# Kernel tuning notes

Hardware: AMD Instinct MI355X
Metric: run time of the kernel (lower is better)

Reference implementation:

```python
import jax, jax.numpy as jnp
import numpy as np

N = 20000      # nodes
E = 320000     # edges
G = 512        # graphs in batch
F_IN = 64      # node_feature_dim
SOLV = 128     # solvent fingerprint dim
OUT = 1        # output_dim
EPS = 1e-5     # BatchNorm eps


def setup_inputs() -> dict:
    key = jax.random.key(0)
    ks = jax.random.split(key, 24)
    inp = {
        'x': jax.random.normal(ks[0], (N, F_IN), jnp.float32),
        'edge_index': jax.random.randint(ks[1], (2, E), 0, N),
        'batch': jnp.sort(jax.random.randint(ks[2], (N,), 0, G)),
        'solvent_fingerprint': jax.random.normal(ks[3], (G, SOLV), jnp.float32),
        # GCNConv 1: 64 -> 128
        'W1': jax.random.normal(ks[4], (F_IN, 128), jnp.float32) / np.sqrt(F_IN),
        'b1': jnp.zeros((128,), jnp.float32),
        'g1': 1.0 + 0.1 * jax.random.normal(ks[5], (128,), jnp.float32),
        'be1': 0.1 * jax.random.normal(ks[6], (128,), jnp.float32),
        # GCNConv 2: 128 -> 256
        'W2': jax.random.normal(ks[7], (128, 256), jnp.float32) / np.sqrt(128),
        'b2': jnp.zeros((256,), jnp.float32),
        'g2': 1.0 + 0.1 * jax.random.normal(ks[8], (256,), jnp.float32),
        'be2': 0.1 * jax.random.normal(ks[9], (256,), jnp.float32),
        # fc_solvent: 128 -> 128
        'Ws': jax.random.normal(ks[10], (SOLV, 128), jnp.float32) / np.sqrt(SOLV),
        'bs': jnp.zeros((128,), jnp.float32),
        # fc1: 384 -> 128 (+ BN)
        'Wf1': jax.random.normal(ks[11], (384, 128), jnp.float32) / np.sqrt(384),
        'bf1': jnp.zeros((128,), jnp.float32),
        'gf1': 1.0 + 0.1 * jax.random.normal(ks[12], (128,), jnp.float32),
        'bef1': 0.1 * jax.random.normal(ks[13], (128,), jnp.float32),
        # fc2: 128 -> OUT
        'Wf2': jax.random.normal(ks[14], (128, OUT), jnp.float32) / np.sqrt(128),
        'bf2': jnp.zeros((OUT,), jnp.float32),
    }
    return inp


def _batchnorm(h, g, b):
    # training-mode BatchNorm1d: biased batch statistics
    mu = jnp.mean(h, axis=0)
    var = jnp.var(h, axis=0)
    return g * (h - mu) * jax.lax.rsqrt(var + EPS) + b


def _gcn_norm(edge_index, n_nodes):
    # add self-loops, symmetric normalization (PyG GCNConv default)
    loops = jnp.arange(n_nodes)
    row = jnp.concatenate([edge_index[0], loops])
    col = jnp.concatenate([edge_index[1], loops])
    deg = jax.ops.segment_sum(jnp.ones_like(col, jnp.float32), col, num_segments=n_nodes)
    dis = jax.lax.rsqrt(deg)  # deg >= 1 due to self-loops
    norm = dis[row] * dis[col]  # [E+N]
    return row, col, norm


def _gcn_conv(h, W, b, row, col, norm, n_nodes):
    hw = h @ W                                   # [N, F_out]
    msg = hw[row] * norm[:, None]                # gather + scale
    agg = jax.ops.segment_sum(msg, col, num_segments=n_nodes)
    return agg + b


def reference(x, edge_index, batch, solvent_fingerprint,
              W1, b1, g1, be1, W2, b2, g2, be2,
              Ws, bs, Wf1, bf1, gf1, bef1, Wf2, bf2):
    n = x.shape[0]
    row, col, norm = _gcn_norm(edge_index, n)

    h = jax.nn.relu(_batchnorm(_gcn_conv(x, W1, b1, row, col, norm, n), g1, be1))
    h = jax.nn.relu(_batchnorm(_gcn_conv(h, W2, b2, row, col, norm, n), g2, be2))

    # global_mean_pool
    sums = jax.ops.segment_sum(h, batch, num_segments=G)
    cnts = jax.ops.segment_sum(jnp.ones((n,), h.dtype), batch, num_segments=G)
    pooled = sums / jnp.maximum(cnts, 1.0)[:, None]          # [G, 256]

    solv = jax.nn.relu(solvent_fingerprint @ Ws + bs)        # [G, 128]
    z = jnp.concatenate([pooled, solv], axis=1)              # [G, 384]
    z = jax.nn.relu(_batchnorm(z @ Wf1 + bf1, gf1, bef1))    # dropout = identity (eval)
    return z @ Wf2 + bf2                                     # [G, OUT]
```

## Files before the change

### kernel.cpp

```cpp
#include <hip/hip_runtime.h>
#include <hip/hip_bf16.h>
#include <hip/hip_fp16.h>

#define EPS 1e-5f
#define CAP 64

typedef __attribute__((ext_vector_type(8))) short short8_t;
typedef __attribute__((ext_vector_type(8))) unsigned short ushort8_t;
typedef __attribute__((ext_vector_type(4))) float f32x4_t;

__device__ inline unsigned short f2bf(float f) {
    unsigned int u = __float_as_uint(f);
    unsigned int r = (u + 0x7FFFu + ((u >> 16) & 1u)) >> 16;
    return (unsigned short)r;
}
__device__ inline float bf2f(unsigned short h) {
    return __uint_as_float((unsigned int)h << 16);
}

__global__ void prep_kernel(const float* __restrict__ x, unsigned short* __restrict__ xb,
                            int* __restrict__ cursor, float* __restrict__ st,
                            const int* __restrict__ batch, int* __restrict__ seg,
                            float* __restrict__ out, const float* __restrict__ bf2,
                            int n, int G) {
    int i = blockIdx.x * blockDim.x + threadIdx.x;
    if (i < n * 8) {
        const float4* xf4 = (const float4*)x;
        float4 u = xf4[i * 2];
        float4 v = xf4[i * 2 + 1];
        ushort8_t h;
        h[0] = f2bf(u.x); h[1] = f2bf(u.y); h[2] = f2bf(u.z); h[3] = f2bf(u.w);
        h[4] = f2bf(v.x); h[5] = f2bf(v.y); h[6] = f2bf(v.z); h[7] = f2bf(v.w);
        ((ushort8_t*)xb)[i] = h;
    }
    if (i < n) cursor[i] = 0;
    if (i < 1028) st[i] = 0.f;
    if (i < G) out[i] = bf2[0];
    if (i <= G) {
        if (i == G) { seg[G] = n; }
        else {
            int lo = 0, hi = n;
            while (lo < hi) {
                int mid = (lo + hi) >> 1;
                if (batch[mid] < i) lo = mid + 1; else hi = mid;
            }
            seg[i] = lo;
        }
    }
}

__global__ void fillb_kernel(const int* __restrict__ ei, int* __restrict__ cursor,
                             unsigned int* __restrict__ recs, int E) {
    int e = blockIdx.x * blockDim.x + threadIdx.x;
    if (e >= E) return;
    int r = ei[e];
    int c = ei[E + e];
    int pos = atomicAdd(&cursor[c], 1);
    recs[(size_t)c * CAP + pos] = (unsigned int)r;
}

__global__ __launch_bounds__(256)
void gather1_pack_kernel(const unsigned short* __restrict__ xb,
                         const int* __restrict__ cursor,
                         unsigned int* __restrict__ recs,
                         unsigned short* __restrict__ dst,
                         int n, int gps, int GB1) {
    const int bid = blockIdx.x;
    const int t   = threadIdx.x;

    if (bid >= GB1) {
        int i = (bid - GB1) * 256 + t;
        int node = i >> 6;
        if (node < n && (i & 63) < cursor[node]) {
            unsigned int r = recs[i] & 0xFFFFu;
            float w = rsqrtf((float)cursor[r] + 1.0f);
            recs[i] = (((unsigned int)__half_as_ushort(__float2half_rn(w))) << 16) | r;
        }
        return;
    }

    int xl    = bid & 7;
    int slice = xl >> 2;
    int group = (bid >> 3) * 4 + (xl & 3);
    if (group >= gps) return;
    int local = t / 4;
    int lane  = t % 4;
    int node  = group * 64 + local;
    if (node >= n) return;
    int f8    = slice * 4 + lane;

    const ushort8_t* src8 = (const ushort8_t*)xb;
    int deg  = cursor[node];
    float di = rsqrtf((float)deg + 1.0f);
    ushort8_t sv = src8[(size_t)node * 8 + f8];
    float acc[8], acc2[8];
#pragma unroll
    for (int j = 0; j < 8; j++) { acc[j] = bf2f(sv[j]) * di; acc2[j] = 0.f; }

    int e  = node * CAP;
    int e1 = e + deg;
    for (; e + 1 < e1; e += 2) {
        int r0 = recs[e] & 0xFFFF;
        int r1 = recs[e + 1] & 0xFFFF;
        float w0 = rsqrtf((float)cursor[r0] + 1.0f);
        float w1 = rsqrtf((float)cursor[r1] + 1.0f);
        ushort8_t v0 = src8[(size_t)r0 * 8 + f8];
        ushort8_t v1 = src8[(size_t)r1 * 8 + f8];
#pragma unroll
        for (int j = 0; j < 8; j++) {
            acc[j]  = fmaf(bf2f(v0[j]), w0, acc[j]);
            acc2[j] = fmaf(bf2f(v1[j]), w1, acc2[j]);
        }
    }
    if (e < e1) {
        int r0 = recs[e] & 0xFFFF;
        float w0 = rsqrtf((float)cursor[r0] + 1.0f);
        ushort8_t v0 = src8[(size_t)r0 * 8 + f8];
#pragma unroll
        for (int j = 0; j < 8; j++) acc[j] = fmaf(bf2f(v0[j]), w0, acc[j]);
    }
    ushort8_t o;
#pragma unroll
    for (int j = 0; j < 8; j++) o[j] = f2bf((acc[j] + acc2[j]) * di);
    ((ushort8_t*)dst)[(size_t)node * 8 + f8] = o;
}

template <int F, bool BN>
__launch_bounds__(256)
__global__ void gather_kernel(const unsigned short* __restrict__ src,
                              const int* __restrict__ cursor,
                              const unsigned int* __restrict__ recs,
                              const float* __restrict__ st, const float* __restrict__ gamma,
                              const float* __restrict__ beta, float inv_n,
                              unsigned short* __restrict__ dst, int n, int gps) {
    constexpr int F8  = F / 8;
    constexpr int W8  = F8 / 2;
    constexpr int NPB = 256 / W8;

    int bid = blockIdx.x;
    int xl  = bid & 7;
    int slice = xl >> 2;
    int group = (bid >> 3) * 4 + (xl & 3);
    if (group >= gps) return;

    int local = threadIdx.x / W8;
    int lane  = threadIdx.x % W8;
    int node  = group * NPB + local;
    if (node >= n) return;
    int f8    = slice * W8 + lane;
    int feat0 = f8 * 8;

    float sc[8], sh[8];
    if (BN) {
#pragma unroll
        for (int j = 0; j < 8; j++) {
            float m = st[feat0 + j] * inv_n;
            float v = st[F + feat0 + j] * inv_n - m * m;
            sc[j] = gamma[feat0 + j] * rsqrtf(v + EPS);
            sh[j] = beta[feat0 + j] - m * sc[j];
        }
    }

    const ushort8_t* src8 = (const ushort8_t*)src;
    int deg  = cursor[node];
    float di = rsqrtf((float)deg + 1.0f);
    ushort8_t sv = src8[(size_t)node * F8 + f8];
    float acc[8], acc2[8];
#pragma unroll
    for (int j = 0; j < 8; j++) {
        float f = bf2f(sv[j]);
        if (BN) f = fmaxf(fmaf(f, sc[j], sh[j]), 0.f);
        acc[j]  = f * di;
        acc2[j] = 0.f;
    }

    int e  = node * CAP;
    int e1 = e + deg;
    for (; e + 1 < e1; e += 2) {
        unsigned int q0 = recs[e], q1 = recs[e + 1];
        int r0 = q0 & 0xFFFF, r1 = q1 & 0xFFFF;
        float w0 = __half2float(__ushort_as_half((unsigned short)(q0 >> 16)));
        float w1 = __half2float(__ushort_as_half((unsigned short)(q1 >> 16)));
        ushort8_t v0 = src8[(size_t)r0 * F8 + f8];
        ushort8_t v1 = src8[(size_t)r1 * F8 + f8];
#pragma unroll
        for (int j = 0; j < 8; j++) {
            float f0 = bf2f(v0[j]);
            float f1 = bf2f(v1[j]);
            if (BN) {
                f0 = fmaxf(fmaf(f0, sc[j], sh[j]), 0.f);
                f1 = fmaxf(fmaf(f1, sc[j], sh[j]), 0.f);
            }
            acc[j]  = fmaf(f0, w0, acc[j]);
            acc2[j] = fmaf(f1, w1, acc2[j]);
        }
    }
    if (e < e1) {
        unsigned int q0 = recs[e];
        int r0 = q0 & 0xFFFF;
        float w0 = __half2float(__ushort_as_half((unsigned short)(q0 >> 16)));
        ushort8_t v0 = src8[(size_t)r0 * F8 + f8];
#pragma unroll
        for (int j = 0; j < 8; j++) {
            float f0 = bf2f(v0[j]);
            if (BN) f0 = fmaxf(fmaf(f0, sc[j], sh[j]), 0.f);
            acc[j] = fmaf(f0, w0, acc[j]);
        }
    }
    ushort8_t o;
#pragma unroll
    for (int j = 0; j < 8; j++) o[j] = f2bf((acc[j] + acc2[j]) * di);
    ((ushort8_t*)dst)[(size_t)node * F8 + f8] = o;
}

template <int K, int NTOT, int OMODE, bool A_F32, bool STATS>
__device__ void gemm_body(char* smemc, int row0, int col0,
                          const void* __restrict__ A, int lda,
                          const float* __restrict__ B, const float* __restrict__ bias,
                          void* __restrict__ Cout, int ldc, float* __restrict__ st, int M) {
    constexpr int KP = K + 8;
    unsigned short (*As)[KP] = (unsigned short (*)[KP])smemc;
    unsigned short (*Bs)[KP] = (unsigned short (*)[KP])(smemc + (size_t)64 * KP * 2);
    float (*sred)[64][2]     = (float (*)[64][2])(smemc + (size_t)2 * 64 * KP * 2);

    const int t    = threadIdx.x;
    const int lane = t & 63;
    const int wave = t >> 6;
    const int wr   = wave >> 1;
    const int wc   = wave & 1;

    constexpr int PA = (64 * K / 8) / 256;
#pragma unroll
    for (int p = 0; p < PA; p++) {
        int fi = t + 256 * p;
        int r  = fi / (K / 8);
        int c8 = fi % (K / 8);
        ushort8_t v = {};
        if (row0 + r < M) {
            if (A_F32) {
                const float* Af = (const float*)A;
                float4 u0 = *(const float4*)&Af[(size_t)(row0 + r) * lda + c8 * 8];
                float4 u1 = *(const float4*)&Af[(size_t)(row0 + r) * lda + c8 * 8 + 4];
                v[0] = f2bf(u0.x); v[1] = f2bf(u0.y); v[2] = f2bf(u0.z); v[3] = f2bf(u0.w);
                v[4] = f2bf(u1.x); v[5] = f2bf(u1.y); v[6] = f2bf(u1.z); v[7] = f2bf(u1.w);
            } else {
                v = *(const ushort8_t*)&((const unsigned short*)A)[(size_t)(row0 + r) * lda + c8 * 8];
            }
        }
        *(ushort8_t*)&As[r][c8 * 8] = v;
    }
    constexpr int PB = (K * 16) / 256;
#pragma unroll
    for (int p = 0; p < PB; p++) {
        int fi = t + 256 * p;
        int k  = fi >> 4;
        int c4 = fi & 15;
        float4 v = *(const float4*)&B[(size_t)k * NTOT + col0 + c4 * 4];
        Bs[c4 * 4 + 0][k] = f2bf(v.x);
        Bs[c4 * 4 + 1][k] = f2bf(v.y);
        Bs[c4 * 4 + 2][k] = f2bf(v.z);
        Bs[c4 * 4 + 3][k] = f2bf(v.w);
    }
    __syncthreads();

    const int l15 = lane & 15;
    const int l16 = lane >> 4;
    f32x4_t acc[2][2] = {};
#pragma unroll
    for (int ks = 0; ks < K / 32; ks++) {
        int koff = ks * 32 + l16 * 8;
        short8_t a0 = *(const short8_t*)&As[wr * 32 + l15][koff];
        short8_t a1 = *(const short8_t*)&As[wr * 32 + 16 + l15][koff];
        short8_t b0 = *(const short8_t*)&Bs[wc * 32 + l15][koff];
        short8_t b1 = *(const short8_t*)&Bs[wc * 32 + 16 + l15][koff];
        acc[0][0] = __builtin_amdgcn_mfma_f32_16x16x32_bf16(a0, b0, acc[0][0], 0, 0, 0);
        acc[0][1] = __builtin_amdgcn_mfma_f32_16x16x32_bf16(a0, b1, acc[0][1], 0, 0, 0);
        acc[1][0] = __builtin_amdgcn_mfma_f32_16x16x32_bf16(a1, b0, acc[1][0], 0, 0, 0);
        acc[1][1] = __builtin_amdgcn_mfma_f32_16x16x32_bf16(a1, b1, acc[1][1], 0, 0, 0);
    }

    float s1[2] = {0.f, 0.f}, s2[2] = {0.f, 0.f};
#pragma unroll
    for (int m = 0; m < 2; m++) {
#pragma unroll
        for (int j = 0; j < 4; j++) {
            int row = row0 + wr * 32 + m * 16 + l16 * 4 + j;
            if (row < M) {
#pragma unroll
                for (int nn = 0; nn < 2; nn++) {
                    int col = col0 + wc * 32 + nn * 16 + l15;
                    float v = acc[m][nn][j] + bias[col];
                    if (OMODE == 2) v = fmaxf(v, 0.f);
                    if (OMODE == 0) ((float*)Cout)[(size_t)row * ldc + col] = v;
                    else ((unsigned short*)Cout)[(size_t)row * ldc + col] = f2bf(v);
                    if (STATS) { s1[nn] += v; s2[nn] += v * v; }
                }
            }
        }
    }
    if (STATS) {
#pragma unroll
        for (int nn = 0; nn < 2; nn++) {
            s1[nn] += __shfl_xor(s1[nn], 16);
            s1[nn] += __shfl_xor(s1[nn], 32);
            s2[nn] += __shfl_xor(s2[nn], 16);
            s2[nn] += __shfl_xor(s2[nn], 32);
        }
        if (lane < 16) {
#pragma unroll
            for (int nn = 0; nn < 2; nn++) {
                sred[wr][wc * 32 + nn * 16 + lane][0] = s1[nn];
                sred[wr][wc * 32 + nn * 16 + lane][1] = s2[nn];
            }
        }
        __syncthreads();
        if (t < 64) {
            float a = sred[0][t][0] + sred[1][t][0];
            float b = sred[0][t][1] + sred[1][t][1];
            atomicAdd(&st[col0 + t], a);
            atomicAdd(&st[NTOT + col0 + t], b);
        }
    }
}

__global__ __launch_bounds__(256)
void gemm1_solv_kernel(const unsigned short* __restrict__ a1b,
                       const float* __restrict__ W1, const float* __restrict__ b1,
                       unsigned short* __restrict__ h1b, float* __restrict__ st1,
                       const float* __restrict__ sf, const float* __restrict__ Ws,
                       const float* __restrict__ bs, unsigned short* __restrict__ zs,
                       int n, int g1b, int G) {
    __shared__ alignas(16) char smem[35840];
    int bid = blockIdx.x;
    if (bid < g1b) {
        int MT = g1b / 2;
        gemm_body<64, 128, 1, false, true>(smem, (bid % MT) * 64, (bid / MT) * 64,
                                           a1b, 64, W1, b1, h1b, 128, st1, n);
    } else {
        int s = bid - g1b;
        gemm_body<128, 128, 2, true, false>(smem, (s >> 1) * 64, (s & 1) * 64,
                                            sf, 128, Ws, bs, zs, 128, nullptr, G);
    }
}

__global__ __launch_bounds__(256)
void gemm2_kernel(const unsigned short* __restrict__ h1, const float* __restrict__ W2,
                  const float* __restrict__ b2, float* __restrict__ a2,
                  float* __restrict__ st2, int n) {
    __shared__ alignas(16) char smem[35840];
    gemm_body<128, 256, 0, false, true>(smem, blockIdx.x * 64, blockIdx.y * 64,
                                        h1, 128, W2, b2, a2, 256, st2, n);
}

__launch_bounds__(256)
__global__ void pool_kernel(const float* __restrict__ a2, const int* __restrict__ seg,
                            const float* __restrict__ st2, const float* __restrict__ g2,
                            const float* __restrict__ be2, float inv_n,
                            unsigned short* __restrict__ z) {
    __shared__ float4 red[4][64];
    int g  = blockIdx.x;
    int t  = threadIdx.x;
    int r  = t >> 6;
    int f4 = t & 63;

    float4 sc, sh;
    {
        float m0 = st2[f4 * 4 + 0] * inv_n, m1 = st2[f4 * 4 + 1] * inv_n;
        float m2 = st2[f4 * 4 + 2] * inv_n, m3 = st2[f4 * 4 + 3] * inv_n;
        sc.x = g2[f4 * 4 + 0] * rsqrtf(st2[256 + f4 * 4 + 0] * inv_n - m0 * m0 + EPS);
        sc.y = g2[f4 * 4 + 1] * rsqrtf(st2[256 + f4 * 4 + 1] * inv_n - m1 * m1 + EPS);
        sc.z = g2[f4 * 4 + 2] * rsqrtf(st2[256 + f4 * 4 + 2] * inv_n - m2 * m2 + EPS);
        sc.w = g2[f4 * 4 + 3] * rsqrtf(st2[256 + f4 * 4 + 3] * inv_n - m3 * m3 + EPS);
        sh.x = be2[f4 * 4 + 0] - m0 * sc.x;
        sh.y = be2[f4 * 4 + 1] - m1 * sc.y;
        sh.z = be2[f4 * 4 + 2] - m2 * sc.z;
        sh.w = be2[f4 * 4 + 3] - m3 * sc.w;
    }

    int i0 = seg[g], i1 = seg[g + 1];
    float4 acc = make_float4(0.f, 0.f, 0.f, 0.f);
    for (int i = i0 + r; i < i1; i += 4) {
        float4 v = *(const float4*)&a2[(size_t)i * 256 + f4 * 4];
        acc.x += fmaxf(fmaf(v.x, sc.x, sh.x), 0.f);
        acc.y += fmaxf(fmaf(v.y, sc.y, sh.y), 0.f);
        acc.z += fmaxf(fmaf(v.z, sc.z, sh.z), 0.f);
        acc.w += fmaxf(fmaf(v.w, sc.w, sh.w), 0.f);
    }
    red[r][f4] = acc;
    __syncthreads();
    if (t < 64) {
        float4 a = red[0][t], b = red[1][t], c = red[2][t], d = red[3][t];
        float inv = 1.0f / fmaxf((float)(i1 - i0), 1.f);
        ushort4 o;
        o.x = f2bf((a.x + b.x + c.x + d.x) * inv);
        o.y = f2bf((a.y + b.y + c.y + d.y) * inv);
        o.z = f2bf((a.z + b.z + c.z + d.z) * inv);
        o.w = f2bf((a.w + b.w + c.w + d.w) * inv);
        *(ushort4*)&z[(size_t)g * 256 + t * 4] = o;
    }
}

__global__ __launch_bounds__(256)
void head_kernel(const unsigned short* __restrict__ z, const unsigned short* __restrict__ zs,
                 const float* __restrict__ Wf1, const float* __restrict__ bf1,
                 const float* __restrict__ gf, const float* __restrict__ bef,
                 const float* __restrict__ Wf2,
                 float* __restrict__ stf, int* __restrict__ ctr,
                 float* __restrict__ out, float inv_g, int nblocks) {
    constexpr int KP = 136;
    __shared__ unsigned short As[64][KP];
    __shared__ unsigned short Bs[64][KP];
    __shared__ float sred[2][64][2];

    const int t    = threadIdx.x;
    const int lane = t & 63;
    const int wave = t >> 6;
    const int wr   = wave >> 1;
    const int wc   = wave & 1;
    const int row0 = (blockIdx.x >> 1) * 64;
    const int col0 = (blockIdx.x & 1) * 64;
    const int l15  = lane & 15;
    const int l16  = lane >> 4;

    f32x4_t acc[2][2] = {};
    for (int kc = 0; kc < 3; kc++) {
        __syncthreads();
#pragma unroll
        for (int p = 0; p < 4; p++) {
            int fi = t + 256 * p;
            int r  = fi >> 4, c8 = fi & 15;
            const unsigned short* ap = (kc < 2)
                ? &z[(size_t)(row0 + r) * 256 + kc * 128 + c8 * 8]
                : &zs[(size_t)(row0 + r) * 128 + c8 * 8];
            *(ushort8_t*)&As[r][c8 * 8] = *(const ushort8_t*)ap;
        }
#pragma unroll
        for (int p = 0; p < 8; p++) {
            int fi = t + 256 * p;
            int k  = fi >> 4, c4 = fi & 15;
            float4 v = *(const float4*)&Wf1[(size_t)(kc * 128 + k) * 128 + col0 + c4 * 4];
            Bs[c4 * 4 + 0][k] = f2bf(v.x);
            Bs[c4 * 4 + 1][k] = f2bf(v.y);
            Bs[c4 * 4 + 2][k] = f2bf(v.z);
            Bs[c4 * 4 + 3][k] = f2bf(v.w);
        }
        __syncthreads();
#pragma unroll
        for (int ks = 0; ks < 4; ks++) {
            int koff = ks * 32 + l16 * 8;
            short8_t a0 = *(const short8_t*)&As[wr * 32 + l15][koff];
            short8_t a1 = *(const short8_t*)&As[wr * 32 + 16 + l15][koff];
            short8_t b0 = *(const short8_t*)&Bs[wc * 32 + l15][koff];
            short8_t b1 = *(const short8_t*)&Bs[wc * 32 + 16 + l15][koff];
            acc[0][0] = __builtin_amdgcn_mfma_f32_16x16x32_bf16(a0, b0, acc[0][0], 0, 0, 0);
            acc[0][1] = __builtin_amdgcn_mfma_f32_16x16x32_bf16(a0, b1, acc[0][1], 0, 0, 0);
            acc[1][0] = __builtin_amdgcn_mfma_f32_16x16x32_bf16(a1, b0, acc[1][0], 0, 0, 0);
            acc[1][1] = __builtin_amdgcn_mfma_f32_16x16x32_bf16(a1, b1, acc[1][1], 0, 0, 0);
        }
    }

    float s1[2] = {0.f, 0.f}, s2[2] = {0.f, 0.f};
#pragma unroll
    for (int m = 0; m < 2; m++)
#pragma unroll
        for (int j = 0; j < 4; j++)
#pragma unroll
            for (int nn = 0; nn < 2; nn++) {
                int col = col0 + wc * 32 + nn * 16 + l15;
                float v = acc[m][nn][j] + bf1[col];
                acc[m][nn][j] = v;
                s1[nn] += v;
                s2[nn] += v * v;
            }
#pragma unroll
    for (int nn = 0; nn < 2; nn++) {
        s1[nn] += __shfl_xor(s1[nn], 16);
        s1[nn] += __shfl_xor(s1[nn], 32);
        s2[nn] += __shfl_xor(s2[nn], 16);
        s2[nn] += __shfl_xor(s2[nn], 32);
    }
    if (lane < 16) {
#pragma unroll
        for (int nn = 0; nn < 2; nn++) {
            sred[wr][wc * 32 + nn * 16 + lane][0] = s1[nn];
            sred[wr][wc * 32 + nn * 16 + lane][1] = s2[nn];
        }
    }
    __syncthreads();
    if (t < 64) {
        atomicAdd(&stf[col0 + t],       sred[0][t][0] + sred[1][t][0]);
        atomicAdd(&stf[128 + col0 + t], sred[0][t][1] + sred[1][t][1]);
    }

    __threadfence();
    __syncthreads();
    if (t == 0) {
        atomicAdd(ctr, 1);
        while (atomicAdd(ctr, 0) < nblocks) { }
    }
    __syncthreads();

    float* sflat = &sred[0][0][0];
    sflat[t] = atomicAdd(&stf[t], 0.f);
    __syncthreads();

#pragma unroll
    for (int m = 0; m < 2; m++)
#pragma unroll
        for (int j = 0; j < 4; j++) {
            float p = 0.f;
#pragma unroll
            for (int nn = 0; nn < 2; nn++) {
                int col = col0 + wc * 32 + nn * 16 + l15;
                float mean = sflat[col] * inv_g;
                float var  = sflat[128 + col] * inv_g - mean * mean;
                float sc   = gf[col] * rsqrtf(var + EPS);
                float sh   = bef[col] - mean * sc;
                p += fmaxf(fmaf(acc[m][nn][j], sc, sh), 0.f) * Wf2[col];
            }
            p += __shfl_xor(p, 1);
            p += __shfl_xor(p, 2);
            p += __shfl_xor(p, 4);
            p += __shfl_xor(p, 8);
            if (l15 == 0) {
                int row = wr * 32 + m * 16 + l16 * 4 + j;
                atomicAdd(&out[row0 + row], p);
            }
        }
}

extern "C" void kernel_launch(void* const* d_in, const int* in_sizes, int n_in,
                              void* d_out, int out_size, void* d_ws, size_t ws_size,
                              hipStream_t stream) {
    const float* x    = (const float*)d_in[0];
    const int*   ei   = (const int*)d_in[1];
    const int*   batch= (const int*)d_in[2];
    const float* sf   = (const float*)d_in[3];
    const float* W1   = (const float*)d_in[4];
    const float* b1   = (const float*)d_in[5];
    const float* g1   = (const float*)d_in[6];
    const float* be1  = (const float*)d_in[7];
    const float* W2   = (const float*)d_in[8];
    const float* b2   = (const float*)d_in[9];
    const float* g2   = (const float*)d_in[10];
    const float* be2  = (const float*)d_in[11];
    const float* Ws   = (const float*)d_in[12];
    const float* bs   = (const float*)d_in[13];
    const float* Wf1  = (const float*)d_in[14];
    const float* bf1  = (const float*)d_in[15];
    const float* gf1  = (const float*)d_in[16];
    const float* bef1 = (const float*)d_in[17];
    const float* Wf2  = (const float*)d_in[18];
    const float* bf2  = (const float*)d_in[19];
    float* out = (float*)d_out;

    const int n = in_sizes[0] / 64;
    const int E = in_sizes[1] / 2;
    const int G = in_sizes[3] / 128;

    float* ws   = (float*)d_ws;
    float* a2   = ws;
    unsigned short* xb  = (unsigned short*)(ws + (size_t)n * 256);
    unsigned short* a1b = (unsigned short*)(ws + (size_t)n * 288);
    unsigned short* h1b = (unsigned short*)(ws + (size_t)n * 352);
    unsigned short* z   = (unsigned short*)(ws + (size_t)n * 416);
    unsigned short* zs  = (unsigned short*)(ws + (size_t)n * 416 + (size_t)G * 128);
    float* st   = ws + (size_t)n * 416 + (size_t)G * 192;
    float* st1  = st;
    float* st2  = st + 256;
    float* stf  = st + 768;
    int*   ctr  = (int*)(st + 1024);
    int*   cursor = (int*)(st + 1028);
    int*   seg    = cursor + n;
    unsigned int* recs = (unsigned int*)(seg + G + 1);

    const float inv_nn = 1.0f / (float)n;
    const float inv_gg = 1.0f / (float)G;

    prep_kernel<<<(n * 8 + 255) / 256, 256, 0, stream>>>(x, xb, cursor, st, batch, seg,
                                                         out, bf2, n, G);
    fillb_kernel<<<(E + 255) / 256, 256, 0, stream>>>(ei, cursor, recs, E);

    {
        int gps = (n + 63) / 64;
        int GB1 = ((gps + 3) / 4) * 8;
        int PB  = (n * CAP + 255) / 256;
        gather1_pack_kernel<<<GB1 + PB, 256, 0, stream>>>(xb, cursor, recs, a1b, n, gps, GB1);
    }

    {
        int MT = (n + 63) / 64;
        gemm1_solv_kernel<<<MT * 2 + (G / 64) * 2, 256, 0, stream>>>(
            a1b, W1, b1, h1b, st1, sf, Ws, bs, zs, n, MT * 2, G);
    }

    {
        int gps = (n + 31) / 32;
        int grid = ((gps + 3) / 4) * 8;
        gather_kernel<128, true><<<grid, 256, 0, stream>>>(
            h1b, cursor, recs, st1, g1, be1, inv_nn, a1b, n, gps);
    }

    gemm2_kernel<<<dim3((n + 63) / 64, 4), 256, 0, stream>>>(a1b, W2, b2, a2, st2, n);

    pool_kernel<<<G, 256, 0, stream>>>(a2, seg, st2, g2, be2, inv_nn, z);

    head_kernel<<<(G / 64) * 2, 256, 0, stream>>>(z, zs, Wf1, bf1, gf1, bef1, Wf2,
                                                  stf, ctr, out, inv_gg, (G / 64) * 2);
}
```

Measured before the change: 115.2 us.

## Fuse GCN neighbor gathers into GEMM kernels and store layer-2 output as bf16

The sparse aggregation of each GCN layer now runs inside the GEMM kernels. Each block aggregates its 64-node tile straight into shared memory and then runs MFMA on it, which removes the separate gather kernels and the global round trips for the aggregated activations. Edge records shrink to 16-bit source indices, and the edge weights are recomputed with rsqrt instead of a packing pass. The layer-2 output goes to a bf16 buffer instead of fp32, which halves the traffic into pooling. In exchange, gemm2 loops over all 256 output columns in one block with fewer blocks, may occupy the GPU less well, and loses some precision.

```diff
diff --git a/kernel.cpp b/kernel.cpp
--- a/kernel.cpp
+++ b/kernel.cpp
@@ -50,167 +50,13 @@
 }
 
 __global__ void fillb_kernel(const int* __restrict__ ei, int* __restrict__ cursor,
-                             unsigned int* __restrict__ recs, int E) {
+                             unsigned short* __restrict__ recs, int E) {
     int e = blockIdx.x * blockDim.x + threadIdx.x;
     if (e >= E) return;
     int r = ei[e];
     int c = ei[E + e];
     int pos = atomicAdd(&cursor[c], 1);
-    recs[(size_t)c * CAP + pos] = (unsigned int)r;
-}
-
-__global__ __launch_bounds__(256)
-void gather1_pack_kernel(const unsigned short* __restrict__ xb,
-                         const int* __restrict__ cursor,
-                         unsigned int* __restrict__ recs,
-                         unsigned short* __restrict__ dst,
-                         int n, int gps, int GB1) {
-    const int bid = blockIdx.x;
-    const int t   = threadIdx.x;
-
-    if (bid >= GB1) {
-        int i = (bid - GB1) * 256 + t;
-        int node = i >> 6;
-        if (node < n && (i & 63) < cursor[node]) {
-            unsigned int r = recs[i] & 0xFFFFu;
-            float w = rsqrtf((float)cursor[r] + 1.0f);
-            recs[i] = (((unsigned int)__half_as_ushort(__float2half_rn(w))) << 16) | r;
-        }
-        return;
-    }
-
-    int xl    = bid & 7;
-    int slice = xl >> 2;
-    int group = (bid >> 3) * 4 + (xl & 3);
-    if (group >= gps) return;
-    int local = t / 4;
-    int lane  = t % 4;
-    int node  = group * 64 + local;
-    if (node >= n) return;
-    int f8    = slice * 4 + lane;
-
-    const ushort8_t* src8 = (const ushort8_t*)xb;
-    int deg  = cursor[node];
-    float di = rsqrtf((float)deg + 1.0f);
-    ushort8_t sv = src8[(size_t)node * 8 + f8];
-    float acc[8], acc2[8];
-#pragma unroll
-    for (int j = 0; j < 8; j++) { acc[j] = bf2f(sv[j]) * di; acc2[j] = 0.f; }
-
-    int e  = node * CAP;
-    int e1 = e + deg;
-    for (; e + 1 < e1; e += 2) {
-        int r0 = recs[e] & 0xFFFF;
-        int r1 = recs[e + 1] & 0xFFFF;
-        float w0 = rsqrtf((float)cursor[r0] + 1.0f);
-        float w1 = rsqrtf((float)cursor[r1] + 1.0f);
-        ushort8_t v0 = src8[(size_t)r0 * 8 + f8];
-        ushort8_t v1 = src8[(size_t)r1 * 8 + f8];
-#pragma unroll
-        for (int j = 0; j < 8; j++) {
-            acc[j]  = fmaf(bf2f(v0[j]), w0, acc[j]);
-            acc2[j] = fmaf(bf2f(v1[j]), w1, acc2[j]);
-        }
-    }
-    if (e < e1) {
-        int r0 = recs[e] & 0xFFFF;
-        float w0 = rsqrtf((float)cursor[r0] + 1.0f);
-        ushort8_t v0 = src8[(size_t)r0 * 8 + f8];
-#pragma unroll
-        for (int j = 0; j < 8; j++) acc[j] = fmaf(bf2f(v0[j]), w0, acc[j]);
-    }
-    ushort8_t o;
-#pragma unroll
-    for (int j = 0; j < 8; j++) o[j] = f2bf((acc[j] + acc2[j]) * di);
-    ((ushort8_t*)dst)[(size_t)node * 8 + f8] = o;
-}
-
-template <int F, bool BN>
-__launch_bounds__(256)
-__global__ void gather_kernel(const unsigned short* __restrict__ src,
-                              const int* __restrict__ cursor,
-                              const unsigned int* __restrict__ recs,
-                              const float* __restrict__ st, const float* __restrict__ gamma,
-                              const float* __restrict__ beta, float inv_n,
-                              unsigned short* __restrict__ dst, int n, int gps) {
-    constexpr int F8  = F / 8;
-    constexpr int W8  = F8 / 2;
-    constexpr int NPB = 256 / W8;
-
-    int bid = blockIdx.x;
-    int xl  = bid & 7;
-    int slice = xl >> 2;
-    int group = (bid >> 3) * 4 + (xl & 3);
-    if (group >= gps) return;
-
-    int local = threadIdx.x / W8;
-    int lane  = threadIdx.x % W8;
-    int node  = group * NPB + local;
-    if (node >= n) return;
-    int f8    = slice * W8 + lane;
-    int feat0 = f8 * 8;
-
-    float sc[8], sh[8];
-    if (BN) {
-#pragma unroll
-        for (int j = 0; j < 8; j++) {
-            float m = st[feat0 + j] * inv_n;
-            float v = st[F + feat0 + j] * inv_n - m * m;
-            sc[j] = gamma[feat0 + j] * rsqrtf(v + EPS);
-            sh[j] = beta[feat0 + j] - m * sc[j];
-        }
-    }
-
-    const ushort8_t* src8 = (const ushort8_t*)src;
-    int deg  = cursor[node];
-    float di = rsqrtf((float)deg + 1.0f);
-    ushort8_t sv = src8[(size_t)node * F8 + f8];
-    float acc[8], acc2[8];
-#pragma unroll
-    for (int j = 0; j < 8; j++) {
-        float f = bf2f(sv[j]);
-        if (BN) f = fmaxf(fmaf(f, sc[j], sh[j]), 0.f);
-        acc[j]  = f * di;
-        acc2[j] = 0.f;
-    }
-
-    int e  = node * CAP;
-    int e1 = e + deg;
-    for (; e + 1 < e1; e += 2) {
-        unsigned int q0 = recs[e], q1 = recs[e + 1];
-        int r0 = q0 & 0xFFFF, r1 = q1 & 0xFFFF;
-        float w0 = __half2float(__ushort_as_half((unsigned short)(q0 >> 16)));
-        float w1 = __half2float(__ushort_as_half((unsigned short)(q1 >> 16)));
-        ushort8_t v0 = src8[(size_t)r0 * F8 + f8];
-        ushort8_t v1 = src8[(size_t)r1 * F8 + f8];
-#pragma unroll
-        for (int j = 0; j < 8; j++) {
-            float f0 = bf2f(v0[j]);
-            float f1 = bf2f(v1[j]);
-            if (BN) {
-                f0 = fmaxf(fmaf(f0, sc[j], sh[j]), 0.f);
-                f1 = fmaxf(fmaf(f1, sc[j], sh[j]), 0.f);
-            }
-            acc[j]  = fmaf(f0, w0, acc[j]);
-            acc2[j] = fmaf(f1, w1, acc2[j]);
-        }
-    }
-    if (e < e1) {
-        unsigned int q0 = recs[e];
-        int r0 = q0 & 0xFFFF;
-        float w0 = __half2float(__ushort_as_half((unsigned short)(q0 >> 16)));
-        ushort8_t v0 = src8[(size_t)r0 * F8 + f8];
-#pragma unroll
-        for (int j = 0; j < 8; j++) {
-            float f0 = bf2f(v0[j]);
-            if (BN) f0 = fmaxf(fmaf(f0, sc[j], sh[j]), 0.f);
-            acc[j] = fmaf(f0, w0, acc[j]);
-        }
-    }
-    ushort8_t o;
-#pragma unroll
-    for (int j = 0; j < 8; j++) o[j] = f2bf((acc[j] + acc2[j]) * di);
-    ((ushort8_t*)dst)[(size_t)node * F8 + f8] = o;
+    recs[(size_t)c * CAP + pos] = (unsigned short)r;
 }
 
 template <int K, int NTOT, int OMODE, bool A_F32, bool STATS>
@@ -324,36 +170,302 @@
 }
 
 __global__ __launch_bounds__(256)
-void gemm1_solv_kernel(const unsigned short* __restrict__ a1b,
-                       const float* __restrict__ W1, const float* __restrict__ b1,
-                       unsigned short* __restrict__ h1b, float* __restrict__ st1,
-                       const float* __restrict__ sf, const float* __restrict__ Ws,
-                       const float* __restrict__ bs, unsigned short* __restrict__ zs,
-                       int n, int g1b, int G) {
+void gemm1f_kernel(const unsigned short* __restrict__ xb, const int* __restrict__ cursor,
+                   const unsigned short* __restrict__ recs,
+                   const float* __restrict__ W1, const float* __restrict__ b1,
+                   unsigned short* __restrict__ h1b, float* __restrict__ st1,
+                   const float* __restrict__ sf, const float* __restrict__ Ws,
+                   const float* __restrict__ bs, unsigned short* __restrict__ zs,
+                   int n, int MT, int G) {
     __shared__ alignas(16) char smem[35840];
-    int bid = blockIdx.x;
-    if (bid < g1b) {
-        int MT = g1b / 2;
-        gemm_body<64, 128, 1, false, true>(smem, (bid % MT) * 64, (bid / MT) * 64,
-                                           a1b, 64, W1, b1, h1b, 128, st1, n);
-    } else {
-        int s = bid - g1b;
+    const int bid = blockIdx.x;
+    const int t   = threadIdx.x;
+
+    if (bid >= MT) {
+        int s = bid - MT;
         gemm_body<128, 128, 2, true, false>(smem, (s >> 1) * 64, (s & 1) * 64,
                                             sf, 128, Ws, bs, zs, 128, nullptr, G);
+        return;
+    }
+
+    constexpr int KP = 72;
+    unsigned short (*As)[KP] = (unsigned short (*)[KP])smem;
+    unsigned short (*Bs)[KP] = (unsigned short (*)[KP])(smem + 9216);
+    float (*sred)[64][2]     = (float (*)[64][2])(smem + 9216 + 18432);
+    const int row0 = bid * 64;
+
+    for (int pp = 0; pp < 2; pp++) {
+        int node  = row0 + pp * 32 + (t >> 3);
+        int lane8 = t & 7;
+        float acc[8] = {}, acc2[8] = {};
+        bool valid = node < n;
+        float di = 0.f;
+        if (valid) {
+            const ushort8_t* src8 = (const ushort8_t*)xb;
+            int deg = cursor[node];
+            di = rsqrtf((float)deg + 1.f);
+            ushort8_t sv = src8[(size_t)node * 8 + lane8];
+#pragma unroll
+            for (int j = 0; j < 8; j++) acc[j] = bf2f(sv[j]) * di;
+            int e = node * CAP, e1 = e + deg;
+            for (; e + 1 < e1; e += 2) {
+                int r0 = recs[e], r1 = recs[e + 1];
+                float w0 = rsqrtf((float)cursor[r0] + 1.f);
+                float w1 = rsqrtf((float)cursor[r1] + 1.f);
+                ushort8_t v0 = src8[(size_t)r0 * 8 + lane8];
+                ushort8_t v1 = src8[(size_t)r1 * 8 + lane8];
+#pragma unroll
+                for (int j = 0; j < 8; j++) {
+                    acc[j]  = fmaf(bf2f(v0[j]), w0, acc[j]);
+                    acc2[j] = fmaf(bf2f(v1[j]), w1, acc2[j]);
+                }
+            }
+            if (e < e1) {
+                int r0 = recs[e];
+                float w0 = rsqrtf((float)cursor[r0] + 1.f);
+                ushort8_t v0 = src8[(size_t)r0 * 8 + lane8];
+#pragma unroll
+                for (int j = 0; j < 8; j++) acc[j] = fmaf(bf2f(v0[j]), w0, acc[j]);
+            }
+        }
+        ushort8_t o = {};
+        if (valid) {
+#pragma unroll
+            for (int j = 0; j < 8; j++) o[j] = f2bf((acc[j] + acc2[j]) * di);
+        }
+        *(ushort8_t*)&As[pp * 32 + (t >> 3)][lane8 * 8] = o;
+    }
+
+#pragma unroll
+    for (int p = 0; p < 8; p++) {
+        int fi = t + 256 * p;
+        int k  = fi >> 5;
+        int c4 = fi & 31;
+        float4 v = *(const float4*)&W1[(size_t)k * 128 + c4 * 4];
+        Bs[c4 * 4 + 0][k] = f2bf(v.x);
+        Bs[c4 * 4 + 1][k] = f2bf(v.y);
+        Bs[c4 * 4 + 2][k] = f2bf(v.z);
+        Bs[c4 * 4 + 3][k] = f2bf(v.w);
+    }
+    __syncthreads();
+
+    const int lane = t & 63, wave = t >> 6, wr = wave >> 1, wc = wave & 1;
+    const int l15 = lane & 15, l16 = lane >> 4;
+    f32x4_t acc[2][2][2] = {};
+#pragma unroll
+    for (int ks = 0; ks < 2; ks++) {
+        int koff = ks * 32 + l16 * 8;
+        short8_t a0 = *(const short8_t*)&As[wr * 32 + l15][koff];
+        short8_t a1 = *(const short8_t*)&As[wr * 32 + 16 + l15][koff];
+#pragma unroll
+        for (int p2 = 0; p2 < 2; p2++) {
+            short8_t b0 = *(const short8_t*)&Bs[p2 * 64 + wc * 32 + l15][koff];
+            short8_t b1 = *(const short8_t*)&Bs[p2 * 64 + wc * 32 + 16 + l15][koff];
+            acc[p2][0][0] = __builtin_amdgcn_mfma_f32_16x16x32_bf16(a0, b0, acc[p2][0][0], 0, 0, 0);
+            acc[p2][0][1] = __builtin_amdgcn_mfma_f32_16x16x32_bf16(a0, b1, acc[p2][0][1], 0, 0, 0);
+            acc[p2][1][0] = __builtin_amdgcn_mfma_f32_16x16x32_bf16(a1, b0, acc[p2][1][0], 0, 0, 0);
+            acc[p2][1][1] = __builtin_amdgcn_mfma_f32_16x16x32_bf16(a1, b1, acc[p2][1][1], 0, 0, 0);
+        }
+    }
+
+    for (int p2 = 0; p2 < 2; p2++) {
+        if (p2) __syncthreads();
+        float s1[2] = {0.f, 0.f}, s2[2] = {0.f, 0.f};
+#pragma unroll
+        for (int m = 0; m < 2; m++)
+#pragma unroll
+            for (int j = 0; j < 4; j++) {
+                int row = row0 + wr * 32 + m * 16 + l16 * 4 + j;
+                if (row < n) {
+#pragma unroll
+                    for (int nn = 0; nn < 2; nn++) {
+                        int col = p2 * 64 + wc * 32 + nn * 16 + l15;
+                        float v = acc[p2][m][nn][j] + b1[col];
+                        h1b[(size_t)row * 128 + col] = f2bf(v);
+                        s1[nn] += v;
+                        s2[nn] += v * v;
+                    }
+                }
+            }
+#pragma unroll
+        for (int nn = 0; nn < 2; nn++) {
+            s1[nn] += __shfl_xor(s1[nn], 16);
+            s1[nn] += __shfl_xor(s1[nn], 32);
+            s2[nn] += __shfl_xor(s2[nn], 16);
+            s2[nn] += __shfl_xor(s2[nn], 32);
+        }
+        if (lane < 16) {
+#pragma unroll
+            for (int nn = 0; nn < 2; nn++) {
+                sred[wr][wc * 32 + nn * 16 + lane][0] = s1[nn];
+                sred[wr][wc * 32 + nn * 16 + lane][1] = s2[nn];
+            }
+        }
+        __syncthreads();
+        if (t < 64) {
+            atomicAdd(&st1[p2 * 64 + t],       sred[0][t][0] + sred[1][t][0]);
+            atomicAdd(&st1[128 + p2 * 64 + t], sred[0][t][1] + sred[1][t][1]);
+        }
     }
 }
 
 __global__ __launch_bounds__(256)
-void gemm2_kernel(const unsigned short* __restrict__ h1, const float* __restrict__ W2,
-                  const float* __restrict__ b2, float* __restrict__ a2,
-                  float* __restrict__ st2, int n) {
-    __shared__ alignas(16) char smem[35840];
-    gemm_body<128, 256, 0, false, true>(smem, blockIdx.x * 64, blockIdx.y * 64,
-                                        h1, 128, W2, b2, a2, 256, st2, n);
+void gemm2f_kernel(const unsigned short* __restrict__ a1, const int* __restrict__ cursor,
+                   const unsigned short* __restrict__ recs,
+                   const float* __restrict__ st1, const float* __restrict__ g1,
+                   const float* __restrict__ be1, float inv_n,
+                   const float* __restrict__ W2, const float* __restrict__ b2,
+                   unsigned short* __restrict__ a2b, float* __restrict__ st2, int n) {
+    constexpr int KP = 136;
+    __shared__ unsigned short As[64][KP];
+    __shared__ unsigned short Bs[64][KP];
+    __shared__ float scs[128], shs[128];
+    __shared__ float sred[2][64][2];
+    const int t    = threadIdx.x;
+    const int row0 = blockIdx.x * 64;
+
+    if (t < 128) {
+        float m   = st1[t] * inv_n;
+        float var = st1[128 + t] * inv_n - m * m;
+        float sc  = g1[t] * rsqrtf(var + EPS);
+        scs[t] = sc;
+        shs[t] = be1[t] - m * sc;
+    }
+    __syncthreads();
+
+    for (int pp = 0; pp < 2; pp++) {
+        int node  = row0 + pp * 32 + (t >> 3);
+        int lane8 = t & 7;
+        int f0    = lane8 * 16;
+        float sc[16], sh[16];
+#pragma unroll
+        for (int j = 0; j < 16; j++) { sc[j] = scs[f0 + j]; sh[j] = shs[f0 + j]; }
+        float acc[16] = {}, acc2[16] = {};
+        bool valid = node < n;
+        float di = 0.f;
+        if (valid) {
+            const ushort8_t* src8 = (const ushort8_t*)a1;
+            int deg = cursor[node];
+            di = rsqrtf((float)deg + 1.f);
+            ushort8_t sv0 = src8[(size_t)node * 16 + lane8 * 2];
+            ushort8_t sv1 = src8[(size_t)node * 16 + lane8 * 2 + 1];
+#pragma unroll
+            for (int j = 0; j < 8; j++) {
+                acc[j]     = fmaxf(fmaf(bf2f(sv0[j]), sc[j],     sh[j]),     0.f) * di;
+                acc[8 + j] = fmaxf(fmaf(bf2f(sv1[j]), sc[8 + j], sh[8 + j]), 0.f) * di;
+            }
+            int e = node * CAP, e1 = e + deg;
+            for (; e + 1 < e1; e += 2) {
+                int r0 = recs[e], r1 = recs[e + 1];
+                float w0 = rsqrtf((float)cursor[r0] + 1.f);
+                float w1 = rsqrtf((float)cursor[r1] + 1.f);
+                ushort8_t u0 = src8[(size_t)r0 * 16 + lane8 * 2];
+                ushort8_t u1 = src8[(size_t)r0 * 16 + lane8 * 2 + 1];
+                ushort8_t u2 = src8[(size_t)r1 * 16 + lane8 * 2];
+                ushort8_t u3 = src8[(size_t)r1 * 16 + lane8 * 2 + 1];
+#pragma unroll
+                for (int j = 0; j < 8; j++) {
+                    acc[j]      = fmaf(fmaxf(fmaf(bf2f(u0[j]), sc[j],     sh[j]),     0.f), w0, acc[j]);
+                    acc[8 + j]  = fmaf(fmaxf(fmaf(bf2f(u1[j]), sc[8 + j], sh[8 + j]), 0.f), w0, acc[8 + j]);
+                    acc2[j]     = fmaf(fmaxf(fmaf(bf2f(u2[j]), sc[j],     sh[j]),     0.f), w1, acc2[j]);
+                    acc2[8 + j] = fmaf(fmaxf(fmaf(bf2f(u3[j]), sc[8 + j], sh[8 + j]), 0.f), w1, acc2[8 + j]);
+                }
+            }
+            if (e < e1) {
+                int r0 = recs[e];
+                float w0 = rsqrtf((float)cursor[r0] + 1.f);
+                ushort8_t u0 = src8[(size_t)r0 * 16 + lane8 * 2];
+                ushort8_t u1 = src8[(size_t)r0 * 16 + lane8 * 2 + 1];
+#pragma unroll
+                for (int j = 0; j < 8; j++) {
+                    acc[j]     = fmaf(fmaxf(fmaf(bf2f(u0[j]), sc[j],     sh[j]),     0.f), w0, acc[j]);
+                    acc[8 + j] = fmaf(fmaxf(fmaf(bf2f(u1[j]), sc[8 + j], sh[8 + j]), 0.f), w0, acc[8 + j]);
+                }
+            }
+        }
+        ushort8_t o0 = {}, o1 = {};
+        if (valid) {
+#pragma unroll
+            for (int j = 0; j < 8; j++) {
+                o0[j] = f2bf((acc[j] + acc2[j]) * di);
+                o1[j] = f2bf((acc[8 + j] + acc2[8 + j]) * di);
+            }
+        }
+        *(ushort8_t*)&As[pp * 32 + (t >> 3)][lane8 * 16]     = o0;
+        *(ushort8_t*)&As[pp * 32 + (t >> 3)][lane8 * 16 + 8] = o1;
+    }
+
+    const int lane = t & 63, wave = t >> 6, wr = wave >> 1, wc = wave & 1;
+    const int l15 = lane & 15, l16 = lane >> 4;
+
+    for (int cc = 0; cc < 4; cc++) {
+        __syncthreads();
+#pragma unroll
+        for (int p = 0; p < 8; p++) {
+            int fi = t + 256 * p;
+            int k  = fi >> 4;
+            int c4 = fi & 15;
+            float4 v = *(const float4*)&W2[(size_t)k * 256 + cc * 64 + c4 * 4];
+            Bs[c4 * 4 + 0][k] = f2bf(v.x);
+            Bs[c4 * 4 + 1][k] = f2bf(v.y);
+            Bs[c4 * 4 + 2][k] = f2bf(v.z);
+            Bs[c4 * 4 + 3][k] = f2bf(v.w);
+        }
+        __syncthreads();
+        f32x4_t acc[2][2] = {};
+#pragma unroll
+        for (int ks = 0; ks < 4; ks++) {
+            int koff = ks * 32 + l16 * 8;
+            short8_t a0 = *(const short8_t*)&As[wr * 32 + l15][koff];
+            short8_t a1 = *(const short8_t*)&As[wr * 32 + 16 + l15][koff];
+            short8_t b0 = *(const short8_t*)&Bs[wc * 32 + l15][koff];
+            short8_t b1 = *(const short8_t*)&Bs[wc * 32 + 16 + l15][koff];
+            acc[0][0] = __builtin_amdgcn_mfma_f32_16x16x32_bf16(a0, b0, acc[0][0], 0, 0, 0);
+            acc[0][1] = __builtin_amdgcn_mfma_f32_16x16x32_bf16(a0, b1, acc[0][1], 0, 0, 0);
+            acc[1][0] = __builtin_amdgcn_mfma_f32_16x16x32_bf16(a1, b0, acc[1][0], 0, 0, 0);
+            acc[1][1] = __builtin_amdgcn_mfma_f32_16x16x32_bf16(a1, b1, acc[1][1], 0, 0, 0);
+        }
+        float s1[2] = {0.f, 0.f}, s2[2] = {0.f, 0.f};
+#pragma unroll
+        for (int m = 0; m < 2; m++)
+#pragma unroll
+            for (int j = 0; j < 4; j++) {
+                int row = row0 + wr * 32 + m * 16 + l16 * 4 + j;
+                if (row < n) {
+#pragma unroll
+                    for (int nn = 0; nn < 2; nn++) {
+                        int col = cc * 64 + wc * 32 + nn * 16 + l15;
+                        float v = acc[m][nn][j] + b2[col];
+                        a2b[(size_t)row * 256 + col] = f2bf(v);
+                        s1[nn] += v;
+                        s2[nn] += v * v;
+                    }
+                }
+            }
+#pragma unroll
+        for (int nn = 0; nn < 2; nn++) {
+            s1[nn] += __shfl_xor(s1[nn], 16);
+            s1[nn] += __shfl_xor(s1[nn], 32);
+            s2[nn] += __shfl_xor(s2[nn], 16);
+            s2[nn] += __shfl_xor(s2[nn], 32);
+        }
+        if (lane < 16) {
+#pragma unroll
+            for (int nn = 0; nn < 2; nn++) {
+                sred[wr][wc * 32 + nn * 16 + lane][0] = s1[nn];
+                sred[wr][wc * 32 + nn * 16 + lane][1] = s2[nn];
+            }
+        }
+        __syncthreads();
+        if (t < 64) {
+            atomicAdd(&st2[cc * 64 + t],       sred[0][t][0] + sred[1][t][0]);
+            atomicAdd(&st2[256 + cc * 64 + t], sred[0][t][1] + sred[1][t][1]);
+        }
+    }
 }
 
 __launch_bounds__(256)
-__global__ void pool_kernel(const float* __restrict__ a2, const int* __restrict__ seg,
+__global__ void pool_kernel(const unsigned short* __restrict__ a2b, const int* __restrict__ seg,
                             const float* __restrict__ st2, const float* __restrict__ g2,
                             const float* __restrict__ be2, float inv_n,
                             unsigned short* __restrict__ z) {
@@ -380,11 +492,11 @@
     int i0 = seg[g], i1 = seg[g + 1];
     float4 acc = make_float4(0.f, 0.f, 0.f, 0.f);
     for (int i = i0 + r; i < i1; i += 4) {
-        float4 v = *(const float4*)&a2[(size_t)i * 256 + f4 * 4];
-        acc.x += fmaxf(fmaf(v.x, sc.x, sh.x), 0.f);
-        acc.y += fmaxf(fmaf(v.y, sc.y, sh.y), 0.f);
-        acc.z += fmaxf(fmaf(v.z, sc.z, sh.z), 0.f);
-        acc.w += fmaxf(fmaf(v.w, sc.w, sh.w), 0.f);
+        ushort4 v = *(const ushort4*)&a2b[(size_t)i * 256 + f4 * 4];
+        acc.x += fmaxf(fmaf(bf2f(v.x), sc.x, sh.x), 0.f);
+        acc.y += fmaxf(fmaf(bf2f(v.y), sc.y, sh.y), 0.f);
+        acc.z += fmaxf(fmaf(bf2f(v.z), sc.z, sh.z), 0.f);
+        acc.w += fmaxf(fmaf(bf2f(v.w), sc.w, sh.w), 0.f);
     }
     red[r][f4] = acc;
     __syncthreads();
@@ -558,52 +670,36 @@
     const int E = in_sizes[1] / 2;
     const int G = in_sizes[3] / 128;
 
-    float* ws   = (float*)d_ws;
-    float* a2   = ws;
-    unsigned short* xb  = (unsigned short*)(ws + (size_t)n * 256);
-    unsigned short* a1b = (unsigned short*)(ws + (size_t)n * 288);
-    unsigned short* h1b = (unsigned short*)(ws + (size_t)n * 352);
-    unsigned short* z   = (unsigned short*)(ws + (size_t)n * 416);
-    unsigned short* zs  = (unsigned short*)(ws + (size_t)n * 416 + (size_t)G * 128);
-    float* st   = ws + (size_t)n * 416 + (size_t)G * 192;
+    float* ws = (float*)d_ws;
+    unsigned short* a2b = (unsigned short*)ws;
+    unsigned short* xb  = (unsigned short*)(ws + (size_t)n * 128);
+    unsigned short* h1b = (unsigned short*)(ws + (size_t)n * 160);
+    unsigned short* z   = (unsigned short*)(ws + (size_t)n * 224);
+    unsigned short* zs  = (unsigned short*)(ws + (size_t)n * 224 + (size_t)G * 128);
+    float* st   = ws + (size_t)n * 224 + (size_t)G * 192;
     float* st1  = st;
     float* st2  = st + 256;
     float* stf  = st + 768;
     int*   ctr  = (int*)(st + 1024);
     int*   cursor = (int*)(st + 1028);
     int*   seg    = cursor + n;
-    unsigned int* recs = (unsigned int*)(seg + G + 1);
+    unsigned short* recs = (unsigned short*)(seg + G + 1);
 
     const float inv_nn = 1.0f / (float)n;
     const float inv_gg = 1.0f / (float)G;
+    const int MT = (n + 63) / 64;
 
     prep_kernel<<<(n * 8 + 255) / 256, 256, 0, stream>>>(x, xb, cursor, st, batch, seg,
                                                          out, bf2, n, G);
     fillb_kernel<<<(E + 255) / 256, 256, 0, stream>>>(ei, cursor, recs, E);
 
-    {
-        int gps = (n + 63) / 64;
-        int GB1 = ((gps + 3) / 4) * 8;
-        int PB  = (n * CAP + 255) / 256;
-        gather1_pack_kernel<<<GB1 + PB, 256, 0, stream>>>(xb, cursor, recs, a1b, n, gps, GB1);
-    }
-
-    {
-        int MT = (n + 63) / 64;
-        gemm1_solv_kernel<<<MT * 2 + (G / 64) * 2, 256, 0, stream>>>(
-            a1b, W1, b1, h1b, st1, sf, Ws, bs, zs, n, MT * 2, G);
-    }
-
-    {
-        int gps = (n + 31) / 32;
-        int grid = ((gps + 3) / 4) * 8;
-        gather_kernel<128, true><<<grid, 256, 0, stream>>>(
-            h1b, cursor, recs, st1, g1, be1, inv_nn, a1b, n, gps);
-    }
-
-    gemm2_kernel<<<dim3((n + 63) / 64, 4), 256, 0, stream>>>(a1b, W2, b2, a2, st2, n);
-
-    pool_kernel<<<G, 256, 0, stream>>>(a2, seg, st2, g2, be2, inv_nn, z);
+    gemm1f_kernel<<<MT + (G / 64) * 2, 256, 0, stream>>>(
+        xb, cursor, recs, W1, b1, h1b, st1, sf, Ws, bs, zs, n, MT, G);
+
+    gemm2f_kernel<<<MT, 256, 0, stream>>>(
+        h1b, cursor, recs, st1, g1, be1, inv_nn, W2, b2, a2b, st2, n);
+
+    pool_kernel<<<G, 256, 0, stream>>>(a2b, seg, st2, g2, be2, inv_nn, z);
 
     head_kernel<<<(G / 64) * 2, 256, 0, stream>>>(z, zs, Wf1, bf1, gf1, bef1, Wf2,
                                                   stf, ctr, out, inv_gg, (G / 64) * 2);
```

New measurement: 120.0 us. 4.2% more time.
